# Kernel tuning notes

Measured on AMD Instinct MI355X. Metric: run time of the kernel, lower is better.

Reference implementation:

```python
import jax, jax.numpy as jnp
import numpy as np

N = 100000      # nodes
E = 1200000     # edges
B = 128         # graphs
H = 64          # hidden
IN_DIM = 64
GN_EPS = 1e-5


def _gin(x, edge_index, w1, b1, w2, b2):
    # GINConv (eps=0): mlp(x + sum_{j in N(i)} x_j)
    agg = jax.ops.segment_sum(x[edge_index[0]], edge_index[1], num_segments=N)
    h = x + agg
    return jax.nn.relu(h @ w1 + b1) @ w2 + b2


def _graph_norm(x, batch, w, b, ms):
    # PyG GraphNorm: out = w * (x - ms*mean) / sqrt(var + eps) + b, per-graph stats
    ones = jnp.ones((x.shape[0],), x.dtype)
    cnt = jnp.maximum(jax.ops.segment_sum(ones, batch, num_segments=B), 1.0)[:, None]
    mean = jax.ops.segment_sum(x, batch, num_segments=B) / cnt
    out = x - ms * mean[batch]
    var = jax.ops.segment_sum(out * out, batch, num_segments=B) / cnt
    return out * (jax.lax.rsqrt(var + GN_EPS)[batch] * w) + b


def setup_inputs() -> dict:
    key = jax.random.key(0)
    ks = jax.random.split(key, 32)
    inp = {
        'x': jax.random.normal(ks[0], (N, IN_DIM), jnp.float32),
        'edge_index': jax.random.randint(ks[1], (2, E), 0, N, dtype=jnp.int32),
        'batch': jnp.sort(jax.random.randint(ks[2], (N,), 0, B, dtype=jnp.int32)),
        'u': jax.random.normal(ks[3], (B, 3), jnp.float32),
    }
    k = 4
    for i in range(3):
        fin = IN_DIM if i == 0 else H
        inp[f'w{i+1}a'] = jax.random.normal(ks[k], (fin, H), jnp.float32) / np.sqrt(fin); k += 1
        inp[f'b{i+1}a'] = jnp.zeros((H,), jnp.float32)
        inp[f'w{i+1}b'] = jax.random.normal(ks[k], (H, H), jnp.float32) / np.sqrt(H); k += 1
        inp[f'b{i+1}b'] = jnp.zeros((H,), jnp.float32)
        inp[f'gn{i+1}_w'] = jnp.ones((H,), jnp.float32)
        inp[f'gn{i+1}_b'] = jnp.zeros((H,), jnp.float32)
        inp[f'gn{i+1}_ms'] = jnp.ones((H,), jnp.float32)
    inp['gate_w'] = jax.random.normal(ks[k], (H, 1), jnp.float32) / np.sqrt(H); k += 1
    inp['gate_b'] = jnp.zeros((1,), jnp.float32)
    inp['hw1'] = jax.random.normal(ks[k], (3 * H + 3, H), jnp.float32) / np.sqrt(3 * H + 3); k += 1
    inp['hb1'] = jnp.zeros((H,), jnp.float32)
    inp['hw2'] = jax.random.normal(ks[k], (H, 1), jnp.float32) / np.sqrt(H); k += 1
    inp['hb2'] = jnp.zeros((1,), jnp.float32)
    return inp


def reference(x, edge_index, batch, u,
              w1a, b1a, w1b, b1b, gn1_w, gn1_b, gn1_ms,
              w2a, b2a, w2b, b2b, gn2_w, gn2_b, gn2_ms,
              w3a, b3a, w3b, b3b, gn3_w, gn3_b, gn3_ms,
              gate_w, gate_b, hw1, hb1, hw2, hb2):
    h1 = jax.nn.relu(_graph_norm(_gin(x, edge_index, w1a, b1a, w1b, b1b), batch, gn1_w, gn1_b, gn1_ms))
    h2 = jax.nn.relu(_graph_norm(_gin(h1, edge_index, w2a, b2a, w2b, b2b), batch, gn2_w, gn2_b, gn2_ms))
    h3 = jax.nn.relu(_graph_norm(_gin(h2, edge_index, w3a, b3a, w3b, b3b), batch, gn3_w, gn3_b, gn3_ms))
    h = h1 + h2 + h3

    # AttentionalAggregation: per-graph softmax over gate logits
    gate = h @ gate_w + gate_b                                      # [N,1]
    m = jax.ops.segment_max(gate, batch, num_segments=B)            # [B,1]
    ex = jnp.exp(gate - m[batch])
    den = jax.ops.segment_sum(ex, batch, num_segments=B)
    att = jax.ops.segment_sum((ex / den[batch]) * h, batch, num_segments=B)

    ones = jnp.ones((h.shape[0],), h.dtype)
    cnt = jnp.maximum(jax.ops.segment_sum(ones, batch, num_segments=B), 1.0)[:, None]
    mean_pool = jax.ops.segment_sum(h, batch, num_segments=B) / cnt
    max_pool = jax.ops.segment_max(h, batch, num_segments=B)

    z = jnp.concatenate([att, mean_pool, max_pool, u], axis=1)       # [B, 3H+3]
    out = jax.nn.relu(z @ hw1 + hb1) @ hw2 + hb2                     # head_cls
    return out.reshape(-1)
```

## Files before the change

### kernel.cpp

```cpp
#include <hip/hip_runtime.h>
#include <math.h>

#define HDIM 64
#define GN_EPS 1e-5f
#define MAXNB 512
#define APITCH 72

typedef __attribute__((ext_vector_type(8))) short bf16x8;
typedef __attribute__((ext_vector_type(4))) float f32x4;

__device__ __forceinline__ int lower_bound_i(const int* a, int n, int key){
  int lo = 0, hi = n;
  while (lo < hi){ int mid = (lo + hi) >> 1; if (a[mid] < key) lo = mid + 1; else hi = mid; }
  return lo;
}

__device__ __forceinline__ unsigned fenc(float x){
  unsigned b = __float_as_uint(x);
  return (b & 0x80000000u) ? ~b : (b | 0x80000000u);
}
__device__ __forceinline__ float fdec(unsigned u){
  unsigned b = (u & 0x80000000u) ? (u ^ 0x80000000u) : ~u;
  return __uint_as_float(b);
}

__device__ __forceinline__ unsigned short f2bf(float f){
  unsigned u = __float_as_uint(f);
  u += 0x7fffu + ((u >> 16) & 1u);
  return (unsigned short)(u >> 16);
}
__device__ __forceinline__ float bf2f(unsigned short h){
  return __uint_as_float(((unsigned)h) << 16);
}

__global__ void k_prep(const int* __restrict__ dst, int* __restrict__ bcount, int E, int NB,
                       const float* __restrict__ Wa0, const float* __restrict__ Wb0,
                       const float* __restrict__ Wa1, const float* __restrict__ Wb1,
                       const float* __restrict__ Wa2, const float* __restrict__ Wb2,
                       short* __restrict__ wbf,
                       const int* __restrict__ batch, int N, int* __restrict__ gs, int B){
  int tid = threadIdx.x;
  if (blockIdx.x < 256){
    __shared__ int lh[MAXNB];
    for (int b = tid; b < NB; b += 256) lh[b] = 0;
    __syncthreads();
    for (int i = blockIdx.x * 256 + tid; i < E; i += 256 * 256)
      atomicAdd(&lh[dst[i] >> 8], 1);
    __syncthreads();
    for (int b = tid; b < NB; b += 256){ int c = lh[b]; if (c) atomicAdd(&bcount[b], c); }
  } else if (blockIdx.x < 262){
    int wi = blockIdx.x - 256;
    const float* Wsrc[6] = {Wa0, Wb0, Wa1, Wb1, Wa2, Wb2};
    const float* W = Wsrc[wi];
    short* hi = wbf + wi * 8192;
    short* lo = hi + 4096;
    for (int i = tid; i < 4096; i += 256){
      int k = i >> 6, j = i & 63;
      float v = W[i];
      unsigned short h = f2bf(v);
      hi[j * 64 + k] = (short)h;
      lo[j * 64 + k] = (short)f2bf(v - bf2f(h));
    }
  } else {
    for (int g = tid; g <= B; g += 256) gs[g] = lower_bound_i(batch, N, g);
  }
}

__global__ void k_bscan(const int* __restrict__ bcount, int* __restrict__ bbase,
                        int* __restrict__ bcursor, int NB){
  __shared__ int sd[MAXNB];
  int tid = threadIdx.x;
  int v = (tid < NB) ? bcount[tid] : 0;
  sd[tid] = v; __syncthreads();
  for (int o = 1; o < MAXNB; o <<= 1){
    int t = (tid >= o) ? sd[tid - o] : 0;
    __syncthreads();
    sd[tid] += t;
    __syncthreads();
  }
  int excl = sd[tid] - v;
  if (tid < NB){ bbase[tid] = excl; bcursor[tid] = excl; }
  if (tid == NB - 1) bbase[NB] = excl + v;
}

#define RCHUNK 8192
__global__ void k_breorder(const int* __restrict__ src, const int* __restrict__ dst,
                           int* __restrict__ bcursor, int2* __restrict__ ebuf, int E, int NB){
  __shared__ int lh[MAXNB];
  __shared__ int lbase[MAXNB];
  int tid = threadIdx.x;
  int c0 = blockIdx.x * RCHUNK;
  for (int b = tid; b < NB; b += 256) lh[b] = 0;
  __syncthreads();
  for (int j = 0; j < RCHUNK / 256; j++){
    int i = c0 + j * 256 + tid;
    if (i < E) atomicAdd(&lh[dst[i] >> 8], 1);
  }
  __syncthreads();
  for (int b = tid; b < NB; b += 256){
    int c = lh[b];
    lbase[b] = c ? atomicAdd(&bcursor[b], c) : 0;
    lh[b] = 0;
  }
  __syncthreads();
  for (int j = 0; j < RCHUNK / 256; j++){
    int i = c0 + j * 256 + tid;
    if (i < E){
      int d = dst[i]; int b = d >> 8;
      int r = atomicAdd(&lh[b], 1);
      ebuf[lbase[b] + r] = make_int2(src[i], d);
    }
  }
}

__global__ void k_bucket_csr(const int2* __restrict__ ebuf, const int* __restrict__ bbase,
                             int* __restrict__ deg, int* __restrict__ offs,
                             int* __restrict__ csr, int N){
  __shared__ int lh[256];
  __shared__ int lsc[256];
  int b = blockIdx.x;
  int lo = b << 8;
  int nn = min(256, N - lo);
  int tid = threadIdx.x;
  lh[tid] = 0; __syncthreads();
  int es = bbase[b], ee = bbase[b + 1];
  for (int i = es + tid; i < ee; i += 256) atomicAdd(&lh[ebuf[i].y - lo], 1);
  __syncthreads();
  int v = lh[tid];
  lsc[tid] = v; __syncthreads();
  for (int o = 1; o < 256; o <<= 1){
    int t = (tid >= o) ? lsc[tid - o] : 0;
    __syncthreads();
    lsc[tid] += t;
    __syncthreads();
  }
  int excl = lsc[tid] - v;
  if (tid < nn){ deg[lo + tid] = v; offs[lo + tid] = es + excl; }
  __syncthreads();
  lh[tid] = es + excl;
  __syncthreads();
  for (int i = es + tid; i < ee; i += 256){
    int2 e = ebuf[i];
    int pos = atomicAdd(&lh[e.y - lo], 1);
    csr[pos] = e.x;
  }
}

__global__ __launch_bounds__(256) void k_agg(
    const float* __restrict__ P, const int* __restrict__ csr,
    const int* __restrict__ offs, const int* __restrict__ deg,
    float* __restrict__ G, int n){
  int tid = threadIdx.x;
  int wave_id = blockIdx.x * 4 + (tid >> 6);
  int lane = tid & 63;
  int sub = lane >> 4, l16 = lane & 15;
  int node = wave_id * 4 + sub;
  bool ok = node < n;
  int st = 0, cnt = 0;
  if (ok){ st = offs[node]; cnt = deg[node]; }
  const float4* Pf4 = (const float4*)P;
  float4 a0 = make_float4(0.f, 0.f, 0.f, 0.f);
  float4 a1 = a0, a2 = a0, a3 = a0;
  if (ok) a0 = Pf4[(size_t)node * 16 + l16];
  int sbase = sub << 4;
  for (int base = 0; base < cnt; base += 16){
    int rem = cnt - base;
    int s = (l16 < rem) ? csr[st + base + l16] : 0;
    int m = min(rem, 16);
    int j = 0;
    for (; j + 4 <= m; j += 4){
      int s0 = __shfl(s, sbase | j);
      int s1 = __shfl(s, sbase | (j + 1));
      int s2 = __shfl(s, sbase | (j + 2));
      int s3 = __shfl(s, sbase | (j + 3));
      float4 v0 = Pf4[(size_t)s0 * 16 + l16];
      float4 v1 = Pf4[(size_t)s1 * 16 + l16];
      float4 v2 = Pf4[(size_t)s2 * 16 + l16];
      float4 v3 = Pf4[(size_t)s3 * 16 + l16];
      a0.x += v0.x; a0.y += v0.y; a0.z += v0.z; a0.w += v0.w;
      a1.x += v1.x; a1.y += v1.y; a1.z += v1.z; a1.w += v1.w;
      a2.x += v2.x; a2.y += v2.y; a2.z += v2.z; a2.w += v2.w;
      a3.x += v3.x; a3.y += v3.y; a3.z += v3.z; a3.w += v3.w;
    }
    for (; j < m; ++j){
      int sj = __shfl(s, sbase | j);
      float4 v = Pf4[(size_t)sj * 16 + l16];
      a0.x += v.x; a0.y += v.y; a0.z += v.z; a0.w += v.w;
    }
  }
  if (ok){
    float4 r;
    r.x = (a0.x + a1.x) + (a2.x + a3.x);
    r.y = (a0.y + a1.y) + (a2.y + a3.y);
    r.z = (a0.z + a1.z) + (a2.z + a3.z);
    r.w = (a0.w + a1.w) + (a2.w + a3.w);
    ((float4*)G)[(size_t)node * 16 + l16] = r;
  }
}

__global__ __launch_bounds__(256, 3) void k_mlp(
    float* __restrict__ G, const int* __restrict__ batch,
    const short* __restrict__ Wall,
    const float* __restrict__ B1, const float* __restrict__ B2,
    float* __restrict__ stats, int N){
  __shared__ short Ws[16384];
  __shared__ short Ah[64 * APITCH];
  __shared__ short Al[64 * APITCH];
  __shared__ float ssum[64], ssq[64];
  int tid = threadIdx.x;

  #pragma unroll
  for (int i = 0; i < 8; i++)
    ((float4*)Ws)[i * 256 + tid] = ((const float4*)Wall)[i * 256 + tid];

  int wv = tid >> 6, lane = tid & 63;
  int quad = lane >> 4, l15 = lane & 15;
  int rbase = wv << 4;
  float bb1[4], bb2[4];
  #pragma unroll
  for (int t = 0; t < 4; t++){ bb1[t] = B1[t * 16 + l15]; bb2[t] = B2[t * 16 + l15]; }

  int tile0 = blockIdx.x << 1;
  float4 r[4], r2[4];
  {
    int tb = tile0 << 6;
    #pragma unroll
    for (int ri = 0; ri < 4; ri++){
      int idx = ri * 256 + tid;
      int node = tb + (idx >> 4), f4 = idx & 15;
      r[ri] = make_float4(0.f, 0.f, 0.f, 0.f);
      if (node < N) r[ri] = ((const float4*)G)[(size_t)node * 16 + f4];
    }
  }

  for (int tt = 0; tt < 2; tt++){
    int t0 = (tile0 + tt) << 6;
    if (t0 >= N) break;

    #pragma unroll
    for (int ri = 0; ri < 4; ri++){
      int idx = ri * 256 + tid;
      int node = idx >> 4, f4 = idx & 15;
      float vv[4] = {r[ri].x, r[ri].y, r[ri].z, r[ri].w};
      short h[4], l[4];
      #pragma unroll
      for (int j = 0; j < 4; j++){
        unsigned short hh = f2bf(vv[j]);
        h[j] = (short)hh;
        l[j] = (short)f2bf(vv[j] - bf2f(hh));
      }
      *(short4*)(Ah + node * APITCH + f4 * 4) = make_short4(h[0], h[1], h[2], h[3]);
      *(short4*)(Al + node * APITCH + f4 * 4) = make_short4(l[0], l[1], l[2], l[3]);
    }
    if (tid < 64){ ssum[tid] = 0.f; ssq[tid] = 0.f; }
    __syncthreads();

    if (tt == 0){
      int tb = (tile0 + 1) << 6;
      #pragma unroll
      for (int ri = 0; ri < 4; ri++){
        int idx = ri * 256 + tid;
        int node = tb + (idx >> 4), f4 = idx & 15;
        r2[ri] = make_float4(0.f, 0.f, 0.f, 0.f);
        if (node < N) r2[ri] = ((const float4*)G)[(size_t)node * 16 + f4];
      }
    }

    f32x4 acc[4];
    #pragma unroll
    for (int t = 0; t < 4; t++) acc[t] = (f32x4){0.f, 0.f, 0.f, 0.f};
    #pragma unroll
    for (int kb = 0; kb < 2; kb++){
      int kk = kb * 32 + quad * 8;
      bf16x8 a_h = *(const bf16x8*)(Ah + (rbase + l15) * APITCH + kk);
      bf16x8 a_l = *(const bf16x8*)(Al + (rbase + l15) * APITCH + kk);
      #pragma unroll
      for (int t = 0; t < 4; t++){
        bf16x8 b_h = *(const bf16x8*)(Ws + (t * 16 + l15) * 64 + kk);
        bf16x8 b_l = *(const bf16x8*)(Ws + 4096 + (t * 16 + l15) * 64 + kk);
        acc[t] = __builtin_amdgcn_mfma_f32_16x16x32_bf16(a_h, b_h, acc[t], 0, 0, 0);
        acc[t] = __builtin_amdgcn_mfma_f32_16x16x32_bf16(a_h, b_l, acc[t], 0, 0, 0);
        acc[t] = __builtin_amdgcn_mfma_f32_16x16x32_bf16(a_l, b_h, acc[t], 0, 0, 0);
      }
    }
    __syncthreads();

    #pragma unroll
    for (int t = 0; t < 4; t++){
      #pragma unroll
      for (int rg = 0; rg < 4; rg++){
        float v = fmaxf(acc[t][rg] + bb1[t], 0.f);
        int row = rbase + quad * 4 + rg;
        int col = t * 16 + l15;
        unsigned short hh = f2bf(v);
        Ah[row * APITCH + col] = (short)hh;
        Al[row * APITCH + col] = (short)f2bf(v - bf2f(hh));
      }
    }
    __syncthreads();

    f32x4 acc2[4];
    #pragma unroll
    for (int t = 0; t < 4; t++) acc2[t] = (f32x4){0.f, 0.f, 0.f, 0.f};
    #pragma unroll
    for (int kb = 0; kb < 2; kb++){
      int kk = kb * 32 + quad * 8;
      bf16x8 a_h = *(const bf16x8*)(Ah + (rbase + l15) * APITCH + kk);
      bf16x8 a_l = *(const bf16x8*)(Al + (rbase + l15) * APITCH + kk);
      #pragma unroll
      for (int t = 0; t < 4; t++){
        bf16x8 b_h = *(const bf16x8*)(Ws + 8192 + (t * 16 + l15) * 64 + kk);
        bf16x8 b_l = *(const bf16x8*)(Ws + 12288 + (t * 16 + l15) * 64 + kk);
        acc2[t] = __builtin_amdgcn_mfma_f32_16x16x32_bf16(a_h, b_h, acc2[t], 0, 0, 0);
        acc2[t] = __builtin_amdgcn_mfma_f32_16x16x32_bf16(a_h, b_l, acc2[t], 0, 0, 0);
        acc2[t] = __builtin_amdgcn_mfma_f32_16x16x32_bf16(a_l, b_h, acc2[t], 0, 0, 0);
      }
    }

    int lastn = min(t0 + 63, N - 1);
    int g0 = batch[t0];
    bool uniform = (batch[lastn] == g0) && (t0 + 63 < N);
    #pragma unroll
    for (int t = 0; t < 4; t++){
      int f = t * 16 + l15;
      float s = 0.f, q = 0.f;
      #pragma unroll
      for (int rg = 0; rg < 4; rg++){
        float v = acc2[t][rg] + bb2[t];
        int node = t0 + rbase + quad * 4 + rg;
        if (node < N) G[(size_t)node * HDIM + f] = v;
        if (uniform){
          s += v; q += v * v;
        } else if (node < N){
          int g = batch[node];
          atomicAdd(&stats[g * 128 + f], v);
          atomicAdd(&stats[g * 128 + 64 + f], v * v);
        }
      }
      if (uniform){
        s += __shfl_xor(s, 16); s += __shfl_xor(s, 32);
        q += __shfl_xor(q, 16); q += __shfl_xor(q, 32);
        if (quad == 0){ atomicAdd(&ssum[f], s); atomicAdd(&ssq[f], q); }
      }
    }
    __syncthreads();
    if (uniform && tid < 64){
      atomicAdd(&stats[g0 * 128 + tid], ssum[tid]);
      atomicAdd(&stats[g0 * 128 + 64 + tid], ssq[tid]);
    }
    #pragma unroll
    for (int ri = 0; ri < 4; ri++) r[ri] = r2[ri];
  }
}

__global__ void k_gn_apply(const float* __restrict__ Y, const int* __restrict__ batch,
                           const float* __restrict__ stats, const int* __restrict__ gs,
                           const float* __restrict__ w, const float* __restrict__ ms,
                           const float* __restrict__ bias,
                           float* __restrict__ C, float* __restrict__ hsum, int n16,
                           int first, int writeC){
  int i = blockIdx.x * blockDim.x + threadIdx.x;
  if (i >= n16) return;
  int node = i >> 4, q = i & 15;
  int g = batch[node];
  float cnt = (float)max(gs[g + 1] - gs[g], 1);
  float4 y  = ((const float4*)Y)[i];
  float4 s1 = ((const float4*)(stats + g * 128))[q];
  float4 s2 = ((const float4*)(stats + g * 128 + 64))[q];
  float4 wv = ((const float4*)w)[q];
  float4 mv = ((const float4*)ms)[q];
  float4 bv = ((const float4*)bias)[q];
  float4 v;
  #define APPLY1(c) { \
    float mean = s1.c / cnt; float ex2 = s2.c / cnt; \
    float var = ex2 - (2.f * mv.c - mv.c * mv.c) * mean * mean; \
    float sc = rsqrtf(var + GN_EPS) * wv.c; \
    v.c = fmaxf((y.c - mv.c * mean) * sc + bv.c, 0.f); }
  APPLY1(x) APPLY1(y) APPLY1(z) APPLY1(w)
  #undef APPLY1
  if (writeC) ((float4*)C)[i] = v;
  if (first){
    ((float4*)hsum)[i] = v;
  } else {
    float4 h = ((float4*)hsum)[i];
    h.x += v.x; h.y += v.y; h.z += v.z; h.w += v.w;
    ((float4*)hsum)[i] = h;
  }
}

#define GN_NPW 32
__global__ void k_pool1(const float* __restrict__ HS, const int* __restrict__ batch,
                        const float* __restrict__ GW, const float* __restrict__ GB,
                        float* __restrict__ sumbuf, unsigned* __restrict__ maxbuf,
                        float* __restrict__ gatebuf, unsigned* __restrict__ gmaxbuf, int n){
  int wave = (int)((blockIdx.x * blockDim.x + threadIdx.x) >> 6);
  int lane = threadIdx.x & 63;
  int s = wave * GN_NPW;
  if (s >= n) return;
  int e = min(s + GN_NPW, n);
  float gwv = GW[lane];
  float gb = GB[0];
  int cur = batch[s];
  float macc = 0.f, xacc = -INFINITY, gmx = -INFINITY;
  for (int nd = s; nd < e; ++nd){
    int g = batch[nd];
    if (g != cur){
      atomicAdd(&sumbuf[cur * 64 + lane], macc);
      atomicMax(&maxbuf[cur * 64 + lane], fenc(xacc));
      if (lane == 0) atomicMax(&gmaxbuf[cur], fenc(gmx));
      macc = 0.f; xacc = -INFINITY; gmx = -INFINITY; cur = g;
    }
    float hv = HS[(size_t)nd * HDIM + lane];
    macc += hv; xacc = fmaxf(xacc, hv);
    float gv = hv * gwv;
    #pragma unroll
    for (int msk = 1; msk < 64; msk <<= 1) gv += __shfl_xor(gv, msk);
    gv += gb;
    if (lane == 0) gatebuf[nd] = gv;
    gmx = fmaxf(gmx, gv);
  }
  atomicAdd(&sumbuf[cur * 64 + lane], macc);
  atomicMax(&maxbuf[cur * 64 + lane], fenc(xacc));
  if (lane == 0) atomicMax(&gmaxbuf[cur], fenc(gmx));
}

__global__ void k_pool2(const float* __restrict__ HS, const int* __restrict__ batch,
                        const float* __restrict__ gatebuf, const unsigned* __restrict__ gmaxbuf,
                        float* __restrict__ attbuf, float* __restrict__ denbuf, int n){
  int wave = (int)((blockIdx.x * blockDim.x + threadIdx.x) >> 6);
  int lane = threadIdx.x & 63;
  int s = wave * GN_NPW;
  if (s >= n) return;
  int e = min(s + GN_NPW, n);
  int cur = batch[s];
  float m = fdec(gmaxbuf[cur]);
  float aacc = 0.f, dacc = 0.f;
  for (int nd = s; nd < e; ++nd){
    int g = batch[nd];
    if (g != cur){
      atomicAdd(&attbuf[cur * 64 + lane], aacc);
      if (lane == 0) atomicAdd(&denbuf[cur], dacc);
      aacc = 0.f; dacc = 0.f; cur = g; m = fdec(gmaxbuf[cur]);
    }
    float ex = expf(gatebuf[nd] - m);
    float hv = HS[(size_t)nd * HDIM + lane];
    aacc += ex * hv; dacc += ex;
  }
  atomicAdd(&attbuf[cur * 64 + lane], aacc);
  if (lane == 0) atomicAdd(&denbuf[cur], dacc);
}

__global__ void k_pool3(const float* __restrict__ attbuf, const float* __restrict__ denbuf,
                        const float* __restrict__ sumbuf, const unsigned* __restrict__ maxbuf,
                        const int* __restrict__ gs, const float* __restrict__ U,
                        const float* __restrict__ HW1, const float* __restrict__ HB1,
                        const float* __restrict__ HW2, const float* __restrict__ HB2,
                        float* __restrict__ out){
  __shared__ float z[200];
  int g = blockIdx.x;
  int tid = threadIdx.x;
  float cnt = (float)max(gs[g + 1] - gs[g], 1);
  float den = denbuf[g];
  z[tid]       = attbuf[g * 64 + tid] / den;
  z[64 + tid]  = sumbuf[g * 64 + tid] / cnt;
  z[128 + tid] = fdec(maxbuf[g * 64 + tid]);
  if (tid < 3) z[192 + tid] = U[g * 3 + tid];
  __syncthreads();
  float acc = HB1[tid];
  for (int k = 0; k < 195; k++) acc += z[k] * HW1[k * 64 + tid];
  float sv = fmaxf(acc, 0.f) * HW2[tid];
  #pragma unroll
  for (int msk = 1; msk < 64; msk <<= 1) sv += __shfl_xor(sv, msk);
  if (tid == 0) out[g] = sv + HB2[0];
}

extern "C" void kernel_launch(void* const* d_in, const int* in_sizes, int n_in,
                              void* d_out, int out_size, void* d_ws, size_t ws_size,
                              hipStream_t stream){
  const float* x     = (const float*)d_in[0];
  const int*   ei    = (const int*)d_in[1];
  const int*   batch = (const int*)d_in[2];
  const float* u     = (const float*)d_in[3];
  const float* W[3][4]; const float* GNp[3][3];
  for (int l = 0; l < 3; l++){
    int base = 4 + l * 7;
    W[l][0]  = (const float*)d_in[base + 0];
    W[l][1]  = (const float*)d_in[base + 1];
    W[l][2]  = (const float*)d_in[base + 2];
    W[l][3]  = (const float*)d_in[base + 3];
    GNp[l][0]= (const float*)d_in[base + 4];
    GNp[l][1]= (const float*)d_in[base + 5];
    GNp[l][2]= (const float*)d_in[base + 6];
  }
  const float* gate_w = (const float*)d_in[25];
  const float* gate_b = (const float*)d_in[26];
  const float* hw1    = (const float*)d_in[27];
  const float* hb1    = (const float*)d_in[28];
  const float* hw2    = (const float*)d_in[29];
  const float* hb2    = (const float*)d_in[30];
  float* out = (float*)d_out;

  int N = in_sizes[0] / HDIM;
  int E = in_sizes[1] / 2;
  int B = in_sizes[3] / 3;
  const int* src = ei;
  const int* dst = ei + E;
  int NB = (N + 255) >> 8;

  char* w8 = (char*)d_ws;
  size_t NH = (size_t)N * HDIM * sizeof(float);
  auto alignup = [](size_t v){ return (v + 255) & ~(size_t)255; };
  size_t off = 0;
  float* hsum    = (float*)(w8 + off); off += alignup(NH);
  float* bufA    = (float*)(w8 + off); off += alignup(NH);
  float* bufB    = (float*)(w8 + off); off += alignup(NH);
  float* G       = (float*)(w8 + off); off += alignup(NH);
  float* gatebuf = (float*)(w8 + off); off += alignup((size_t)N * 4);
  int*   deg     = (int*)(w8 + off);   off += alignup((size_t)N * 4);
  int*   offs    = (int*)(w8 + off);   off += alignup((size_t)N * 4);
  int*   csr     = (int*)(w8 + off);   off += alignup((size_t)E * 4);
  int2*  ebuf    = (int2*)(w8 + off);  off += alignup((size_t)E * 8);
  int*   bcount  = (int*)(w8 + off);   off += alignup((size_t)(MAXNB + 1) * 4);
  int*   bbase   = (int*)(w8 + off);   off += alignup((size_t)(MAXNB + 1) * 4);
  int*   bcursor = (int*)(w8 + off);   off += alignup((size_t)(MAXNB + 1) * 4);
  float* stats   = (float*)(w8 + off); off += alignup((size_t)3 * B * 128 * 4);
  float* poolz   = (float*)(w8 + off);
  size_t poolz_bytes = ((size_t)B * 64 * 3 + 2 * B) * 4;
  off += alignup(poolz_bytes);
  float*    sumbuf  = poolz;
  unsigned* maxbuf  = (unsigned*)(poolz + (size_t)B * 64);
  float*    attbuf  = poolz + (size_t)2 * B * 64;
  float*    denbuf  = poolz + (size_t)3 * B * 64;
  unsigned* gmaxbuf = (unsigned*)(poolz + (size_t)3 * B * 64 + B);
  int*   gs      = (int*)(w8 + off);   off += alignup((size_t)(B + 1) * 4);
  short* wbf     = (short*)(w8 + off); off += alignup((size_t)6 * 8192 * 2);
  (void)ws_size; (void)n_in; (void)out_size;

  hipMemsetAsync(stats, 0, (size_t)3 * B * 128 * 4, stream);
  hipMemsetAsync(poolz, 0, poolz_bytes, stream);
  hipMemsetAsync(bcount, 0, (size_t)(MAXNB + 1) * 4, stream);

  const int tb = 256;
  k_prep<<<263, tb, 0, stream>>>(dst, bcount, E, NB,
                                 W[0][0], W[0][2], W[1][0], W[1][2], W[2][0], W[2][2],
                                 wbf, batch, N, gs, B);
  k_bscan<<<1, MAXNB, 0, stream>>>(bcount, bbase, bcursor, NB);
  k_breorder<<<(E + RCHUNK - 1) / RCHUNK, tb, 0, stream>>>(src, dst, bcursor, ebuf, E, NB);
  k_bucket_csr<<<NB, tb, 0, stream>>>(ebuf, bbase, deg, offs, csr, N);

  int nwaves = (N + GN_NPW - 1) / GN_NPW;
  int segblocks = (nwaves * 64 + tb - 1) / tb;
  int n16 = N * 16;
  int nblk64 = (N + 63) >> 6;
  int nblk2 = (nblk64 + 1) >> 1;
  int aggwaves = (N + 3) >> 2;
  int aggblocks = (aggwaves + 3) >> 2;

  const float* P = x;
  float* C = bufA;
  for (int l = 0; l < 3; l++){
    k_agg<<<aggblocks, 256, 0, stream>>>(P, csr, offs, deg, G, N);
    float* lstats = stats + (size_t)l * B * 128;
    k_mlp<<<nblk2, 256, 0, stream>>>(G, batch, wbf + (size_t)l * 16384,
                                     W[l][1], W[l][3], lstats, N);
    k_gn_apply<<<(n16 + tb - 1) / tb, tb, 0, stream>>>(G, batch, lstats, gs,
                                                       GNp[l][0], GNp[l][2], GNp[l][1],
                                                       C, hsum, n16, l == 0 ? 1 : 0,
                                                       l == 2 ? 0 : 1);
    P = C;
    C = (l == 0) ? bufB : bufA;
  }
  k_pool1<<<segblocks, tb, 0, stream>>>(hsum, batch, gate_w, gate_b,
                                        sumbuf, maxbuf, gatebuf, gmaxbuf, N);
  k_pool2<<<segblocks, tb, 0, stream>>>(hsum, batch, gatebuf, gmaxbuf, attbuf, denbuf, N);
  k_pool3<<<B, 64, 0, stream>>>(attbuf, denbuf, sumbuf, maxbuf, gs, u,
                                hw1, hb1, hw2, hb2, out);
}
```

Before: 548.8 us.

## Store node features in bf16 for neighbor gather in aggregation

Adds a conversion kernel that turns the input features into bf16, and has GraphNorm write the next layer's input as bf16. The aggregation kernel now gathers 16-byte bf16 rows with 8 lanes per node and accumulates in fp32, halving the gathered bytes per edge. This targets the memory-bound random gather over 1.2M edges. In exchange it loses input precision in the aggregated sums and adds one extra conversion pass over x.

```diff
diff --git a/kernel.cpp b/kernel.cpp
--- a/kernel.cpp
+++ b/kernel.cpp
@@ -31,6 +31,17 @@
 }
 __device__ __forceinline__ float bf2f(unsigned short h){
   return __uint_as_float(((unsigned)h) << 16);
+}
+
+__device__ __forceinline__ void addbf(float* a, uint4 v){
+  a[0] += __uint_as_float(v.x << 16);
+  a[1] += __uint_as_float(v.x & 0xffff0000u);
+  a[2] += __uint_as_float(v.y << 16);
+  a[3] += __uint_as_float(v.y & 0xffff0000u);
+  a[4] += __uint_as_float(v.z << 16);
+  a[5] += __uint_as_float(v.z & 0xffff0000u);
+  a[6] += __uint_as_float(v.w << 16);
+  a[7] += __uint_as_float(v.w & 0xffff0000u);
 }
 
 __global__ void k_prep(const int* __restrict__ dst, int* __restrict__ bcount, int E, int NB,
@@ -66,6 +77,15 @@
   }
 }
 
+__global__ void k_cvt(const float* __restrict__ x, unsigned short* __restrict__ xb, int n16){
+  int i = blockIdx.x * blockDim.x + threadIdx.x;
+  if (i >= n16) return;
+  float4 v = ((const float4*)x)[i];
+  ushort4 o;
+  o.x = f2bf(v.x); o.y = f2bf(v.y); o.z = f2bf(v.z); o.w = f2bf(v.w);
+  ((ushort4*)xb)[i] = o;
+}
+
 __global__ void k_bscan(const int* __restrict__ bcount, int* __restrict__ bbase,
                         int* __restrict__ bcursor, int NB){
   __shared__ int sd[MAXNB];
@@ -147,54 +167,48 @@
 }
 
 __global__ __launch_bounds__(256) void k_agg(
-    const float* __restrict__ P, const int* __restrict__ csr,
+    const unsigned short* __restrict__ Pb, const int* __restrict__ csr,
     const int* __restrict__ offs, const int* __restrict__ deg,
     float* __restrict__ G, int n){
   int tid = threadIdx.x;
   int wave_id = blockIdx.x * 4 + (tid >> 6);
   int lane = tid & 63;
-  int sub = lane >> 4, l16 = lane & 15;
-  int node = wave_id * 4 + sub;
+  int sub = lane >> 3, l8 = lane & 7;
+  int node = wave_id * 8 + sub;
   bool ok = node < n;
   int st = 0, cnt = 0;
   if (ok){ st = offs[node]; cnt = deg[node]; }
-  const float4* Pf4 = (const float4*)P;
-  float4 a0 = make_float4(0.f, 0.f, 0.f, 0.f);
-  float4 a1 = a0, a2 = a0, a3 = a0;
-  if (ok) a0 = Pf4[(size_t)node * 16 + l16];
-  int sbase = sub << 4;
-  for (int base = 0; base < cnt; base += 16){
+  const uint4* Pv = (const uint4*)Pb;
+  float a[8];
+  #pragma unroll
+  for (int k = 0; k < 8; k++) a[k] = 0.f;
+  if (ok) addbf(a, Pv[(size_t)node * 8 + l8]);
+  int sbase = sub << 3;
+  for (int base = 0; base < cnt; base += 8){
     int rem = cnt - base;
-    int s = (l16 < rem) ? csr[st + base + l16] : 0;
-    int m = min(rem, 16);
+    int s = (l8 < rem) ? csr[st + base + l8] : 0;
+    int m = min(rem, 8);
     int j = 0;
     for (; j + 4 <= m; j += 4){
       int s0 = __shfl(s, sbase | j);
       int s1 = __shfl(s, sbase | (j + 1));
       int s2 = __shfl(s, sbase | (j + 2));
       int s3 = __shfl(s, sbase | (j + 3));
-      float4 v0 = Pf4[(size_t)s0 * 16 + l16];
-      float4 v1 = Pf4[(size_t)s1 * 16 + l16];
-      float4 v2 = Pf4[(size_t)s2 * 16 + l16];
-      float4 v3 = Pf4[(size_t)s3 * 16 + l16];
-      a0.x += v0.x; a0.y += v0.y; a0.z += v0.z; a0.w += v0.w;
-      a1.x += v1.x; a1.y += v1.y; a1.z += v1.z; a1.w += v1.w;
-      a2.x += v2.x; a2.y += v2.y; a2.z += v2.z; a2.w += v2.w;
-      a3.x += v3.x; a3.y += v3.y; a3.z += v3.z; a3.w += v3.w;
+      uint4 v0 = Pv[(size_t)s0 * 8 + l8];
+      uint4 v1 = Pv[(size_t)s1 * 8 + l8];
+      uint4 v2 = Pv[(size_t)s2 * 8 + l8];
+      uint4 v3 = Pv[(size_t)s3 * 8 + l8];
+      addbf(a, v0); addbf(a, v1); addbf(a, v2); addbf(a, v3);
     }
     for (; j < m; ++j){
       int sj = __shfl(s, sbase | j);
-      float4 v = Pf4[(size_t)sj * 16 + l16];
-      a0.x += v.x; a0.y += v.y; a0.z += v.z; a0.w += v.w;
+      addbf(a, Pv[(size_t)sj * 8 + l8]);
     }
   }
   if (ok){
-    float4 r;
-    r.x = (a0.x + a1.x) + (a2.x + a3.x);
-    r.y = (a0.y + a1.y) + (a2.y + a3.y);
-    r.z = (a0.z + a1.z) + (a2.z + a3.z);
-    r.w = (a0.w + a1.w) + (a2.w + a3.w);
-    ((float4*)G)[(size_t)node * 16 + l16] = r;
+    float4* Gp = (float4*)(G + (size_t)node * HDIM + l8 * 8);
+    Gp[0] = make_float4(a[0], a[1], a[2], a[3]);
+    Gp[1] = make_float4(a[4], a[5], a[6], a[7]);
   }
 }
 
@@ -357,7 +371,7 @@
                            const float* __restrict__ stats, const int* __restrict__ gs,
                            const float* __restrict__ w, const float* __restrict__ ms,
                            const float* __restrict__ bias,
-                           float* __restrict__ C, float* __restrict__ hsum, int n16,
+                           unsigned short* __restrict__ Cb, float* __restrict__ hsum, int n16,
                            int first, int writeC){
   int i = blockIdx.x * blockDim.x + threadIdx.x;
   if (i >= n16) return;
@@ -378,7 +392,11 @@
     v.c = fmaxf((y.c - mv.c * mean) * sc + bv.c, 0.f); }
   APPLY1(x) APPLY1(y) APPLY1(z) APPLY1(w)
   #undef APPLY1
-  if (writeC) ((float4*)C)[i] = v;
+  if (writeC){
+    ushort4 o;
+    o.x = f2bf(v.x); o.y = f2bf(v.y); o.z = f2bf(v.z); o.w = f2bf(v.w);
+    ((ushort4*)Cb)[i] = o;
+  }
   if (first){
     ((float4*)hsum)[i] = v;
   } else {
@@ -509,12 +527,14 @@
 
   char* w8 = (char*)d_ws;
   size_t NH = (size_t)N * HDIM * sizeof(float);
+  size_t NHb = (size_t)N * HDIM * sizeof(short);
   auto alignup = [](size_t v){ return (v + 255) & ~(size_t)255; };
   size_t off = 0;
   float* hsum    = (float*)(w8 + off); off += alignup(NH);
-  float* bufA    = (float*)(w8 + off); off += alignup(NH);
-  float* bufB    = (float*)(w8 + off); off += alignup(NH);
   float* G       = (float*)(w8 + off); off += alignup(NH);
+  unsigned short* xb   = (unsigned short*)(w8 + off); off += alignup(NHb);
+  unsigned short* bufA = (unsigned short*)(w8 + off); off += alignup(NHb);
+  unsigned short* bufB = (unsigned short*)(w8 + off); off += alignup(NHb);
   float* gatebuf = (float*)(w8 + off); off += alignup((size_t)N * 4);
   int*   deg     = (int*)(w8 + off);   off += alignup((size_t)N * 4);
   int*   offs    = (int*)(w8 + off);   off += alignup((size_t)N * 4);
@@ -541,23 +561,24 @@
   hipMemsetAsync(bcount, 0, (size_t)(MAXNB + 1) * 4, stream);
 
   const int tb = 256;
+  int n16 = N * 16;
   k_prep<<<263, tb, 0, stream>>>(dst, bcount, E, NB,
                                  W[0][0], W[0][2], W[1][0], W[1][2], W[2][0], W[2][2],
                                  wbf, batch, N, gs, B);
+  k_cvt<<<(n16 + tb - 1) / tb, tb, 0, stream>>>(x, xb, n16);
   k_bscan<<<1, MAXNB, 0, stream>>>(bcount, bbase, bcursor, NB);
   k_breorder<<<(E + RCHUNK - 1) / RCHUNK, tb, 0, stream>>>(src, dst, bcursor, ebuf, E, NB);
   k_bucket_csr<<<NB, tb, 0, stream>>>(ebuf, bbase, deg, offs, csr, N);
 
   int nwaves = (N + GN_NPW - 1) / GN_NPW;
   int segblocks = (nwaves * 64 + tb - 1) / tb;
-  int n16 = N * 16;
   int nblk64 = (N + 63) >> 6;
   int nblk2 = (nblk64 + 1) >> 1;
-  int aggwaves = (N + 3) >> 2;
+  int aggwaves = (N + 7) >> 3;
   int aggblocks = (aggwaves + 3) >> 2;
 
-  const float* P = x;
-  float* C = bufA;
+  const unsigned short* P = xb;
+  unsigned short* C = bufA;
   for (int l = 0; l < 3; l++){
     k_agg<<<aggblocks, 256, 0, stream>>>(P, csr, offs, deg, G, N);
     float* lstats = stats + (size_t)l * B * 128;
```

New measurement: 496.1 us. 1.11x faster.
